# Kernel tuning notes

Measured on AMD Instinct MI355X. Metric: run time of the kernel, lower is better.

## Reference

```python
import jax, jax.numpy as jnp
import numpy as np

NBINS = (128, 64, 32)
LOG2PI = float(np.log(2.0 * np.pi))


def _quadratic_spline_stack(x, genes_oi, local_gene_ix, delta, uh, uw):
    """Stack of piecewise-quadratic (piecewise-linear density) splines on [0,1].
    Per split with n heights / n-1 widths (n-1 bins). Returns (outputs, logabsdet)."""
    uh_oi = uh[genes_oi]  # [G, sum(n)]
    uw_oi = uw[genes_oi]  # [G, sum(n-1)]
    outputs = x
    logabsdet = jnp.zeros_like(x)
    oh = ow = od = 0
    for n in NBINS:
        nh, nw = n, n - 1
        uhs = uh_oi[:, oh:oh + nh]
        uws = uw_oi[:, ow:ow + nw]
        ds = delta[:, od:od + nh]
        oh += nh; ow += nw; od += nh
        # per-gene bin widths / locations
        widths_g = jax.nn.softmax(uws, axis=-1)                     # [G, nw]
        bl = jnp.cumsum(widths_g, axis=-1)
        bl = bl.at[:, -1].set(1.0)
        bin_loc_g = jnp.pad(bl, ((0, 0), (1, 0)))                   # [G, nw+1]
        # gather per cut
        w = widths_g[local_gene_ix]                                 # [N, nw]
        loc = bin_loc_g[local_gene_ix]                              # [N, nw+1]
        # per-cut knot heights: gene baseline + cell/gene delta, normalized to unit area
        h_un = jnp.exp(uhs[local_gene_ix] + ds)                     # [N, nh]
        area = jnp.sum(0.5 * (h_un[:, :-1] + h_un[:, 1:]) * w, axis=-1, keepdims=True)
        h = h_un / area                                             # [N, nh]
        seg = 0.5 * (h[:, :-1] + h[:, 1:]) * w                      # bin masses [N, nw]
        left_cdf = jnp.pad(jnp.cumsum(seg, axis=-1)[:, :-1], ((0, 0), (1, 0)))  # [N, nw]
        # locate bin
        bin_idx = jnp.clip(jnp.sum(outputs[:, None] >= loc, axis=-1) - 1, 0, nw - 1)
        gi = bin_idx[:, None]
        loc_l = jnp.take_along_axis(loc, gi, -1)[:, 0]
        w_b = jnp.take_along_axis(w, gi, -1)[:, 0]
        cdf_l = jnp.take_along_axis(left_cdf, gi, -1)[:, 0]
        h_l = jnp.take_along_axis(h, gi, -1)[:, 0]
        h_r = jnp.take_along_axis(h, gi + 1, -1)[:, 0]
        alpha = (outputs - loc_l) / w_b
        outputs = (0.5 * (h_r - h_l) * w_b) * alpha * alpha + h_l * w_b * alpha + cdf_l
        logabsdet = logabsdet + jnp.log(h_l + (h_r - h_l) * alpha)
    return outputs, logabsdet


def setup_inputs() -> dict:
    key = jax.random.key(0)
    ks = jax.random.split(key, 10)
    B, L, G_total, G_oi, C, N = 512, 16, 20000, 500, 224, 200000
    clustering = jax.random.uniform(ks[0], (B, L), dtype=jnp.float32)
    coordinates = jax.random.uniform(ks[1], (N,), dtype=jnp.float32, minval=1e-4, maxval=1.0 - 1e-4)
    genes_oi = jax.random.randint(ks[2], (G_oi,), 0, G_total)
    local_gene_ix = jax.random.randint(ks[3], (N,), 0, G_oi)
    local_cellxgene_ix = jax.random.randint(ks[4], (N,), 0, B * G_oi)
    localcellxgene_ix = jax.random.randint(ks[5], (N,), 0, B * G_total)
    logit_weight = jax.random.normal(ks[6], (G_total, L, C), dtype=jnp.float32) * 0.01
    rho_weight = jax.random.normal(ks[7], (G_total, L), dtype=jnp.float32) * 0.05
    rho_bias = 1e-5 + (1.0 - 1e-5) * jax.random.uniform(ks[8], (G_total,), dtype=jnp.float32)
    k9, k10 = jax.random.split(ks[9])
    unnormalized_heights = jax.random.normal(k9, (G_total, sum(NBINS)), dtype=jnp.float32) * 0.1
    unnormalized_widths = jax.random.normal(k10, (G_total, sum(n - 1 for n in NBINS)), dtype=jnp.float32) * 0.1
    return dict(clustering=clustering, coordinates=coordinates, genes_oi=genes_oi,
                local_gene_ix=local_gene_ix, local_cellxgene_ix=local_cellxgene_ix,
                localcellxgene_ix=localcellxgene_ix, logit_weight=logit_weight,
                rho_weight=rho_weight, rho_bias=rho_bias,
                unnormalized_heights=unnormalized_heights,
                unnormalized_widths=unnormalized_widths)


def reference(clustering, coordinates, genes_oi, local_gene_ix, local_cellxgene_ix,
              localcellxgene_ix, logit_weight, rho_weight, rho_bias,
              unnormalized_heights, unnormalized_widths):
    B = clustering.shape[0]
    G = genes_oi.shape[0]
    n_total_genes = rho_bias.shape[0]
    # Decoder (n_layers=0 -> nn_output = latent)
    lw_oi = logit_weight[genes_oi]                                   # [G, L, C]
    mixture_delta = jnp.einsum('bl,glc->bgc', clustering, lw_oi)     # [B, G, C]
    rho_delta = clustering @ rho_weight.T                            # [B, G_total]
    rho = jax.nn.softmax(jnp.log(rho_bias)[None, :] + rho_delta, axis=-1)
    rho_cuts = rho.reshape(-1)[localcellxgene_ix]                    # [N]
    md_cuts = mixture_delta.reshape(B * G, -1)[local_cellxgene_ix]   # [N, C]
    _, lik_mixture = _quadratic_spline_stack(coordinates, genes_oi, local_gene_ix,
                                             md_cuts, unnormalized_heights, unnormalized_widths)
    lik_overall = jnp.log(rho_cuts) + jnp.log(jnp.float32(n_total_genes))
    elbo = -jnp.sum(lik_mixture + lik_overall)
    # Normal(0, exp(log_scale=0)=1) regularization log-probs
    def normal_logpdf(v):
        return -0.5 * v * v - 0.5 * LOG2PI
    elbo = elbo - jnp.sum(normal_logpdf(lw_oi))
    elbo = elbo - jnp.sum(normal_logpdf(rho_weight[genes_oi]))
    return elbo
```

## Files before the change

### kernel.cpp

```cpp
#include <hip/hip_runtime.h>
#include <cstddef>

#define LOG2PI_F 1.8378770664093453f

__device__ __forceinline__ float wave_sum(float v) {
#pragma unroll
    for (int o = 32; o >= 1; o >>= 1) v += __shfl_xor(v, o, 64);
    return v;
}

__global__ void k_logrb(const float* __restrict__ rho_bias, float* __restrict__ logrb, int G_total) {
    int g = blockIdx.x * blockDim.x + threadIdx.x;
    if (g < G_total) logrb[g] = __logf(rho_bias[g]);
}

__global__ void k_prep_genes(const int* __restrict__ genes_oi,
                             const float* __restrict__ uh, const float* __restrict__ uw,
                             float* __restrict__ uh_sel, float* __restrict__ w_ws,
                             float* __restrict__ loc_ws) {
    const int g = blockIdx.x;
    const int t = threadIdx.x;
    const int gs = genes_oi[g];

    for (int c = t; c < 224; c += 64) uh_sel[(size_t)g * 224 + c] = uh[(size_t)gs * 224 + c];

    __shared__ float w_s[128];
    int oh = 0, ow = 0;
    const int NH[3] = {128, 64, 32};
    for (int lev = 0; lev < 3; ++lev) {
        const int nh = NH[lev], nw = nh - 1;
        float v0 = (t < nw)      ? uw[(size_t)gs * 221 + ow + t]      : -INFINITY;
        float v1 = (t + 64 < nw) ? uw[(size_t)gs * 221 + ow + t + 64] : -INFINITY;
        float mx = fmaxf(v0, v1);
#pragma unroll
        for (int o = 32; o >= 1; o >>= 1) mx = fmaxf(mx, __shfl_xor(mx, o, 64));
        float e0 = (t < nw)      ? __expf(v0 - mx) : 0.f;
        float e1 = (t + 64 < nw) ? __expf(v1 - mx) : 0.f;
        float sm = wave_sum(e0 + e1);
        float inv = 1.0f / sm;
        float w0 = e0 * inv, w1 = e1 * inv;
        if (t < nw)      { w_s[t]      = w0; w_ws[(size_t)g * 221 + ow + t]      = w0; }
        if (t + 64 < nw) { w_s[t + 64] = w1; w_ws[(size_t)g * 221 + ow + t + 64] = w1; }
        __syncthreads();
        for (int k = t; k < nh; k += 64) {
            float acc = 0.f;
            for (int j = 0; j < k; ++j) acc += w_s[j];
            loc_ws[(size_t)g * 224 + oh + k] = (k == nh - 1) ? 1.0f : acc;
        }
        __syncthreads();
        oh += nh; ow += nw;
    }
}

__global__ void k_prep_lwT(const int* __restrict__ genes_oi,
                           const float* __restrict__ lw, const float* __restrict__ rw,
                           float* __restrict__ lwT, float* __restrict__ pB) {
    const int g = blockIdx.x;
    const int tid = threadIdx.x;
    const int gs = genes_oi[g];
    const float* src = lw + (size_t)gs * 3584;
    float* dst = lwT + (size_t)g * 3584;
    float acc = 0.f;
    if (tid < 224) {
        float vv[16];
#pragma unroll
        for (int l = 0; l < 16; ++l) {
            float v = src[l * 224 + tid];
            vv[l] = v;
            acc = fmaf(v, v, acc);
        }
        float4* d4 = (float4*)(dst + (size_t)tid * 16);
#pragma unroll
        for (int q = 0; q < 4; ++q)
            d4[q] = make_float4(vv[4 * q + 0], vv[4 * q + 1], vv[4 * q + 2], vv[4 * q + 3]);
    }
    if (tid < 16) { float v = rw[(size_t)gs * 16 + tid]; acc = fmaf(v, v, acc); }
    __shared__ float sm[256];
    sm[tid] = acc;
    __syncthreads();
    for (int o = 128; o > 0; o >>= 1) { if (tid < o) sm[tid] += sm[tid + o]; __syncthreads(); }
    if (tid == 0) pB[g] = 0.5f * sm[0] + 0.5f * LOG2PI_F * (3584.0f + 16.0f);
}

__global__ void k_lse(const float* __restrict__ clustering, const float* __restrict__ rw,
                      const float* __restrict__ logrb, float* __restrict__ lse, int G_total) {
    const int b = blockIdx.x;
    const int tid = threadIdx.x;
    __shared__ float cl_s[16];
    if (tid < 16) cl_s[tid] = clustering[(size_t)b * 16 + tid];
    __syncthreads();
    float m = -INFINITY, s = 0.f;
    for (int g = tid; g < G_total; g += blockDim.x) {
        const float4* r4 = (const float4*)(rw + (size_t)g * 16);
        float d = 0.f;
#pragma unroll
        for (int q = 0; q < 4; ++q) {
            float4 v = r4[q];
            d = fmaf(cl_s[4 * q + 0], v.x, d);
            d = fmaf(cl_s[4 * q + 1], v.y, d);
            d = fmaf(cl_s[4 * q + 2], v.z, d);
            d = fmaf(cl_s[4 * q + 3], v.w, d);
        }
        float logit = logrb[g] + d;
        float mn = fmaxf(m, logit);
        s = s * __expf(m - mn) + __expf(logit - mn);
        m = mn;
    }
    __shared__ float ms[256], ss[256];
    ms[tid] = m; ss[tid] = s;
    __syncthreads();
    for (int o = 128; o > 0; o >>= 1) {
        if (tid < o) {
            float m2 = ms[tid + o], s2 = ss[tid + o];
            float mn = fmaxf(ms[tid], m2);
            ss[tid] = ss[tid] * __expf(ms[tid] - mn) + s2 * __expf(m2 - mn);
            ms[tid] = mn;
        }
        __syncthreads();
    }
    if (tid == 0) lse[b] = ms[0] + __logf(ss[0]);
}

__launch_bounds__(256)
__global__ void k_main(const float* __restrict__ coordinates,
                       const int* __restrict__ local_gene_ix,
                       const int* __restrict__ local_cellxgene_ix,
                       const int* __restrict__ localcellxgene_ix,
                       const float* __restrict__ clustering,
                       const float* __restrict__ lwT,
                       const float* __restrict__ rw,
                       const float* __restrict__ logrb,
                       const float* __restrict__ lse,
                       const float* __restrict__ uh_sel,
                       const float* __restrict__ w_ws,
                       const float* __restrict__ loc_ws,
                       float* __restrict__ pA,
                       int N, int G_oi, int G_total) {
    const int tid  = threadIdx.x;
    const int lane = tid & 63;
    const int wid  = tid >> 6;
    const int wglobal = blockIdx.x * 4 + wid;
    const int wstride = gridDim.x * 4;
    const float logGt = __logf((float)G_total);

    float acc = 0.f;

    for (int i = wglobal; i < N; i += wstride) {
        const float x_in = coordinates[i];
        const int g_h = local_gene_ix[i];
        const int lcx = local_cellxgene_ix[i];
        const int lc2 = localcellxgene_ix[i];
        const unsigned b1 = (unsigned)lcx / (unsigned)G_oi;
        const unsigned gm = (unsigned)lcx - b1 * (unsigned)G_oi;
        const unsigned b2 = (unsigned)lc2 / (unsigned)G_total;
        const unsigned gt = (unsigned)lc2 - b2 * (unsigned)G_total;

        float cl[16];
        {
            const float4* c4 = (const float4*)(clustering + (size_t)b1 * 16);
#pragma unroll
            for (int q = 0; q < 4; ++q) {
                float4 v = c4[q];
                cl[4 * q + 0] = v.x; cl[4 * q + 1] = v.y; cl[4 * q + 2] = v.z; cl[4 * q + 3] = v.w;
            }
        }

        const float* lwtg = lwT   + (size_t)gm  * 3584;
        const float* uhg  = uh_sel + (size_t)g_h * 224;
        const float* wg   = w_ws   + (size_t)g_h * 221;
        const float* lg   = loc_ws + (size_t)g_h * 224;

        float x = x_in;
        float lad = 0.f;
        int oh = 0, ow = 0;
        const int NH[3] = {128, 64, 32};
#pragma unroll
        for (int lev = 0; lev < 3; ++lev) {
            const int n = NH[lev];
            const int c0 = lane, c1 = lane + 64;
            const bool a0 = (c0 < n);
            const bool a1 = (n > 64);
            float h0 = 0.f, h1 = 0.f;
            if (a0) {
                const float4* p4 = (const float4*)(lwtg + (size_t)(oh + c0) * 16);
                float d = 0.f;
#pragma unroll
                for (int q = 0; q < 4; ++q) {
                    float4 v = p4[q];
                    d = fmaf(cl[4 * q + 0], v.x, d);
                    d = fmaf(cl[4 * q + 1], v.y, d);
                    d = fmaf(cl[4 * q + 2], v.z, d);
                    d = fmaf(cl[4 * q + 3], v.w, d);
                }
                h0 = __expf(uhg[oh + c0] + d);
            }
            if (a1) {
                const float4* p4 = (const float4*)(lwtg + (size_t)(oh + c1) * 16);
                float d = 0.f;
#pragma unroll
                for (int q = 0; q < 4; ++q) {
                    float4 v = p4[q];
                    d = fmaf(cl[4 * q + 0], v.x, d);
                    d = fmaf(cl[4 * q + 1], v.y, d);
                    d = fmaf(cl[4 * q + 2], v.z, d);
                    d = fmaf(cl[4 * q + 3], v.w, d);
                }
                h1 = __expf(uhg[oh + c1] + d);
            }
            const float h0n = __shfl(h0, (lane + 1) & 63, 64);
            const float h1n = __shfl(h1, (lane + 1) & 63, 64);
            const float h64 = __shfl(h1, 0, 64);

            float segA = 0.f, segB = 0.f;
            if (lane < n - 1) {
                float hr = (lane < 63) ? h0n : h64;
                segA = 0.5f * (h0 + hr) * wg[ow + lane];
            }
            if (a1 && lane < 63) {
                segB = 0.5f * (h1 + h1n) * wg[ow + lane + 64];
            }

            float loc0 = a0 ? lg[oh + c0] : 2.f;
            float loc1 = a1 ? lg[oh + c1] : 2.f;
            unsigned long long bb0 = __ballot(a0 && (x >= loc0));
            unsigned long long bb1 = __ballot(a1 && (x >= loc1));
            int cnt = __popcll(bb0) + __popcll(bb1);
            int bi = min(max(cnt - 1, 0), n - 2);

            float pref = ((lane < bi) ? segA : 0.f) + (((lane + 64) < bi) ? segB : 0.f);
            float area = wave_sum(segA + segB);
            float cdf_raw = wave_sum(pref);

            float hl  = (bi < 64)     ? __shfl(h0, bi, 64)     : __shfl(h1, bi - 64, 64);
            int bip = bi + 1;
            float hr2 = (bip < 64)    ? __shfl(h0, bip, 64)    : __shfl(h1, bip - 64, 64);

            float inv_area = 1.0f / area;
            float loc_l = lg[oh + bi];
            float w_b   = wg[ow + bi];
            float hlr = hl * inv_area, hrr = hr2 * inv_area;
            float alpha = (x - loc_l) / w_b;
            x = 0.5f * (hrr - hlr) * w_b * alpha * alpha + hlr * w_b * alpha + cdf_raw * inv_area;
            lad += __logf(hlr + (hrr - hlr) * alpha);
            oh += n; ow += n - 1;
        }

        float d2 = 0.f;
        {
            const float4* c4 = (const float4*)(clustering + (size_t)b2 * 16);
            const float4* r4 = (const float4*)(rw + (size_t)gt * 16);
#pragma unroll
            for (int q = 0; q < 4; ++q) {
                float4 cv = c4[q], rv = r4[q];
                d2 = fmaf(cv.x, rv.x, d2);
                d2 = fmaf(cv.y, rv.y, d2);
                d2 = fmaf(cv.z, rv.z, d2);
                d2 = fmaf(cv.w, rv.w, d2);
            }
        }
        float lik_ov = logrb[gt] + d2 - lse[b2] + logGt;
        acc += -(lad + lik_ov);
    }

    __shared__ float wsum[4];
    if (lane == 0) wsum[wid] = acc;
    __syncthreads();
    if (tid == 0) pA[blockIdx.x] = wsum[0] + wsum[1] + wsum[2] + wsum[3];
}

__global__ void k_final(const float* __restrict__ pA, const float* __restrict__ pB,
                        float* __restrict__ out, int nA, int nB) {
    const int tid = threadIdx.x;
    float acc = 0.f;
    for (int i = tid; i < nA; i += blockDim.x) acc += pA[i];
    for (int i = tid; i < nB; i += blockDim.x) acc += pB[i];
    __shared__ float sm[256];
    sm[tid] = acc;
    __syncthreads();
    for (int o = 128; o > 0; o >>= 1) { if (tid < o) sm[tid] += sm[tid + o]; __syncthreads(); }
    if (tid == 0) out[0] = sm[0];
}

extern "C" void kernel_launch(void* const* d_in, const int* in_sizes, int n_in,
                              void* d_out, int out_size, void* d_ws, size_t ws_size,
                              hipStream_t stream) {
    const float* clustering        = (const float*)d_in[0];
    const float* coordinates       = (const float*)d_in[1];
    const int*   genes_oi          = (const int*)d_in[2];
    const int*   local_gene_ix     = (const int*)d_in[3];
    const int*   local_cellxgene_ix= (const int*)d_in[4];
    const int*   localcellxgene_ix = (const int*)d_in[5];
    const float* lw                = (const float*)d_in[6];
    const float* rw                = (const float*)d_in[7];
    const float* rho_bias          = (const float*)d_in[8];
    const float* uh                = (const float*)d_in[9];
    const float* uw                = (const float*)d_in[10];

    const int G_total = in_sizes[8];
    const int G_oi    = in_sizes[2];
    const int N       = in_sizes[1];
    const int L       = in_sizes[7] / G_total;
    const int B       = in_sizes[0] / L;
    (void)L;

    const int NBLK = 2048;

    size_t off = 0;
    float* base = (float*)d_ws;
    auto alloc = [&](size_t nfloats) {
        float* p = base + off;
        off += (nfloats + 3) & ~(size_t)3;
        return p;
    };
    float* pA      = alloc(NBLK);
    float* pB      = alloc(G_oi);
    float* lse     = alloc(B);
    float* logrb   = alloc(G_total);
    float* lwT     = alloc((size_t)G_oi * 3584);
    float* uh_sel  = alloc((size_t)G_oi * 224);
    float* w_ws    = alloc((size_t)G_oi * 221);
    float* loc_ws  = alloc((size_t)G_oi * 224);
    (void)ws_size;

    k_logrb<<<(G_total + 255) / 256, 256, 0, stream>>>(rho_bias, logrb, G_total);
    k_prep_genes<<<G_oi, 64, 0, stream>>>(genes_oi, uh, uw, uh_sel, w_ws, loc_ws);
    k_prep_lwT<<<G_oi, 256, 0, stream>>>(genes_oi, lw, rw, lwT, pB);
    k_lse<<<B, 256, 0, stream>>>(clustering, rw, logrb, lse, G_total);
    k_main<<<NBLK, 256, 0, stream>>>(coordinates, local_gene_ix, local_cellxgene_ix,
                                     localcellxgene_ix, clustering, lwT, rw, logrb, lse,
                                     uh_sel, w_ws, loc_ws, pA, N, G_oi, G_total);
    k_final<<<1, 256, 0, stream>>>(pA, pB, (float*)d_out, NBLK, G_oi);
}
```

Baseline: 744.8 us.

## Bucket cuts by gene and evaluate spline per-thread with sequential bin scan

Replaces the one-wave-per-cut spline evaluation with a counting sort of cuts by mixture gene (histogram, scan, scatter) followed by one block per gene, where each thread walks all bins of a cut serially. Gene-side data (heights, half-widths, knot locations) is packed into float4 records and the knot cumulative sum becomes a wave scan. This removes the per-cut cross-lane shuffles and reductions and lets a block share one gene's weight rows through cache. In exchange each thread does about 220 serial dot products and exps, there are several extra launches with atomics, and load balance now depends on how many cuts each gene has.

```diff
diff --git a/kernel.cpp b/kernel.cpp
--- a/kernel.cpp
+++ b/kernel.cpp
@@ -6,6 +6,19 @@
 __device__ __forceinline__ float wave_sum(float v) {
 #pragma unroll
     for (int o = 32; o >= 1; o >>= 1) v += __shfl_xor(v, o, 64);
+    return v;
+}
+__device__ __forceinline__ float wave_max(float v) {
+#pragma unroll
+    for (int o = 32; o >= 1; o >>= 1) v = fmaxf(v, __shfl_xor(v, o, 64));
+    return v;
+}
+__device__ __forceinline__ float wave_scan_incl(float v, int lane) {
+#pragma unroll
+    for (int o = 1; o < 64; o <<= 1) {
+        float t = __shfl_up(v, o, 64);
+        if (lane >= o) v += t;
+    }
     return v;
 }
 
@@ -16,40 +29,42 @@
 
 __global__ void k_prep_genes(const int* __restrict__ genes_oi,
                              const float* __restrict__ uh, const float* __restrict__ uw,
-                             float* __restrict__ uh_sel, float* __restrict__ w_ws,
-                             float* __restrict__ loc_ws) {
+                             float4* __restrict__ pk) {
     const int g = blockIdx.x;
     const int t = threadIdx.x;
     const int gs = genes_oi[g];
-
-    for (int c = t; c < 224; c += 64) uh_sel[(size_t)g * 224 + c] = uh[(size_t)gs * 224 + c];
-
-    __shared__ float w_s[128];
-    int oh = 0, ow = 0;
+    const float* uhg = uh + (size_t)gs * 224;
+    const float* uwg = uw + (size_t)gs * 221;
+    float4* pkg = pk + (size_t)g * 224;
+
     const int NH[3] = {128, 64, 32};
+    const int OH[3] = {0, 128, 192};
+    const int OW[3] = {0, 127, 190};
+    const int SO[3] = {0, 128, 191};
+#pragma unroll
     for (int lev = 0; lev < 3; ++lev) {
-        const int nh = NH[lev], nw = nh - 1;
-        float v0 = (t < nw)      ? uw[(size_t)gs * 221 + ow + t]      : -INFINITY;
-        float v1 = (t + 64 < nw) ? uw[(size_t)gs * 221 + ow + t + 64] : -INFINITY;
-        float mx = fmaxf(v0, v1);
-#pragma unroll
-        for (int o = 32; o >= 1; o >>= 1) mx = fmaxf(mx, __shfl_xor(mx, o, 64));
+        const int nw = NH[lev] - 1;
+        float v0 = (t < nw)      ? uwg[OW[lev] + t]      : -INFINITY;
+        float v1 = (t + 64 < nw) ? uwg[OW[lev] + t + 64] : -INFINITY;
+        float mx = wave_max(fmaxf(v0, v1));
         float e0 = (t < nw)      ? __expf(v0 - mx) : 0.f;
         float e1 = (t + 64 < nw) ? __expf(v1 - mx) : 0.f;
-        float sm = wave_sum(e0 + e1);
-        float inv = 1.0f / sm;
+        float inv = 1.0f / wave_sum(e0 + e1);
         float w0 = e0 * inv, w1 = e1 * inv;
-        if (t < nw)      { w_s[t]      = w0; w_ws[(size_t)g * 221 + ow + t]      = w0; }
-        if (t + 64 < nw) { w_s[t + 64] = w1; w_ws[(size_t)g * 221 + ow + t + 64] = w1; }
-        __syncthreads();
-        for (int k = t; k < nh; k += 64) {
-            float acc = 0.f;
-            for (int j = 0; j < k; ++j) acc += w_s[j];
-            loc_ws[(size_t)g * 224 + oh + k] = (k == nh - 1) ? 1.0f : acc;
-        }
-        __syncthreads();
-        oh += nh; ow += nw;
-    }
+        float i0 = wave_scan_incl(w0, t);
+        float tot0 = __shfl(i0, 63, 64);
+        float i1 = wave_scan_incl(w1, t) + tot0;
+        if (t < nw) {
+            float loc = (t == nw - 1) ? 1.0f : i0;
+            pkg[SO[lev] + t] = make_float4(uhg[OH[lev] + t + 1], 0.5f * w0, loc, 0.f);
+        }
+        if (t + 64 < nw) {
+            int j = t + 64;
+            float loc = (j == nw - 1) ? 1.0f : i1;
+            pkg[SO[lev] + j] = make_float4(uhg[OH[lev] + j + 1], 0.5f * w1, loc, 0.f);
+        }
+    }
+    if (t == 0) pkg[127] = make_float4(uhg[0], uhg[128], uhg[192], 0.f);
 }
 
 __global__ void k_prep_lwT(const int* __restrict__ genes_oi,
@@ -121,39 +136,79 @@
     if (tid == 0) lse[b] = ms[0] + __logf(ss[0]);
 }
 
-__launch_bounds__(256)
-__global__ void k_main(const float* __restrict__ coordinates,
-                       const int* __restrict__ local_gene_ix,
-                       const int* __restrict__ local_cellxgene_ix,
-                       const int* __restrict__ localcellxgene_ix,
-                       const float* __restrict__ clustering,
-                       const float* __restrict__ lwT,
-                       const float* __restrict__ rw,
-                       const float* __restrict__ logrb,
-                       const float* __restrict__ lse,
-                       const float* __restrict__ uh_sel,
-                       const float* __restrict__ w_ws,
-                       const float* __restrict__ loc_ws,
-                       float* __restrict__ pA,
-                       int N, int G_oi, int G_total) {
-    const int tid  = threadIdx.x;
-    const int lane = tid & 63;
-    const int wid  = tid >> 6;
-    const int wglobal = blockIdx.x * 4 + wid;
-    const int wstride = gridDim.x * 4;
+__global__ void k_zero(int* __restrict__ p, int n) {
+    int i = blockIdx.x * blockDim.x + threadIdx.x;
+    if (i < n) p[i] = 0;
+}
+
+__global__ void k_hist(const int* __restrict__ lcx, int* __restrict__ counts, int N, int G_oi) {
+    int i = blockIdx.x * blockDim.x + threadIdx.x;
+    if (i < N) atomicAdd(&counts[(unsigned)lcx[i] % (unsigned)G_oi], 1);
+}
+
+__global__ void k_scan(const int* __restrict__ counts, int* __restrict__ offsets,
+                       int* __restrict__ cursor, int G_oi) {
+    __shared__ int sm[512];
+    const int t = threadIdx.x;
+    int v = (t < G_oi) ? counts[t] : 0;
+    sm[t] = v;
+    __syncthreads();
+    for (int o = 1; o < 512; o <<= 1) {
+        int add = (t >= o) ? sm[t - o] : 0;
+        __syncthreads();
+        sm[t] += add;
+        __syncthreads();
+    }
+    if (t < G_oi) {
+        offsets[t + 1] = sm[t];
+        cursor[t] = sm[t] - v;
+    }
+    if (t == 0) offsets[0] = 0;
+}
+
+__global__ void k_scatter(const float* __restrict__ coord, const int* __restrict__ lgix,
+                          const int* __restrict__ lcx, const int* __restrict__ lc2,
+                          int* __restrict__ cursor,
+                          float* __restrict__ xs, int* __restrict__ b1s,
+                          int* __restrict__ lc2s, int* __restrict__ ghs, int N, int G_oi) {
+    int i = blockIdx.x * blockDim.x + threadIdx.x;
+    if (i >= N) return;
+    unsigned v = (unsigned)lcx[i];
+    unsigned g = v % (unsigned)G_oi;
+    int pos = atomicAdd(&cursor[g], 1);
+    xs[pos]   = coord[i];
+    b1s[pos]  = (int)(v / (unsigned)G_oi);
+    lc2s[pos] = lc2[i];
+    ghs[pos]  = lgix[i];
+}
+
+__launch_bounds__(512, 4)
+__global__ void k_main2(const float* __restrict__ xs, const int* __restrict__ b1s,
+                        const int* __restrict__ lc2s, const int* __restrict__ ghs,
+                        const int* __restrict__ offsets,
+                        const float* __restrict__ clustering,
+                        const float* __restrict__ lwT,
+                        const float4* __restrict__ pk,
+                        const float* __restrict__ rw,
+                        const float* __restrict__ logrb,
+                        const float* __restrict__ lse,
+                        float* __restrict__ pA, int G_oi, int G_total) {
+    const int g = blockIdx.x;
+    const int tid = threadIdx.x;
+    const float* lwg = lwT + (size_t)g * 3584;
+    const int s = offsets[g], e = offsets[g + 1];
     const float logGt = __logf((float)G_total);
-
     float acc = 0.f;
 
-    for (int i = wglobal; i < N; i += wstride) {
-        const float x_in = coordinates[i];
-        const int g_h = local_gene_ix[i];
-        const int lcx = local_cellxgene_ix[i];
-        const int lc2 = localcellxgene_ix[i];
-        const unsigned b1 = (unsigned)lcx / (unsigned)G_oi;
-        const unsigned gm = (unsigned)lcx - b1 * (unsigned)G_oi;
-        const unsigned b2 = (unsigned)lc2 / (unsigned)G_total;
-        const unsigned gt = (unsigned)lc2 - b2 * (unsigned)G_total;
+    for (int base = s; base < e; base += 512) {
+        const int i = base + tid;
+        const bool valid = i < e;
+        const int isafe = valid ? i : s;
+        float x = xs[isafe];
+        const int b1  = b1s[isafe];
+        const int lc2 = lc2s[isafe];
+        const int gh  = ghs[isafe];
+        const float4* pkh = pk + (size_t)gh * 224;
 
         float cl[16];
         {
@@ -164,108 +219,76 @@
                 cl[4 * q + 0] = v.x; cl[4 * q + 1] = v.y; cl[4 * q + 2] = v.z; cl[4 * q + 3] = v.w;
             }
         }
-
-        const float* lwtg = lwT   + (size_t)gm  * 3584;
-        const float* uhg  = uh_sel + (size_t)g_h * 224;
-        const float* wg   = w_ws   + (size_t)g_h * 221;
-        const float* lg   = loc_ws + (size_t)g_h * 224;
-
-        float x = x_in;
+        const float4 uh0 = pkh[127];
+        const float uh0v[3] = {uh0.x, uh0.y, uh0.z};
+
         float lad = 0.f;
-        int oh = 0, ow = 0;
         const int NH[3] = {128, 64, 32};
+        const int OH[3] = {0, 128, 192};
+        const int SO[3] = {0, 128, 191};
 #pragma unroll
         for (int lev = 0; lev < 3; ++lev) {
-            const int n = NH[lev];
-            const int c0 = lane, c1 = lane + 64;
-            const bool a0 = (c0 < n);
-            const bool a1 = (n > 64);
-            float h0 = 0.f, h1 = 0.f;
-            if (a0) {
-                const float4* p4 = (const float4*)(lwtg + (size_t)(oh + c0) * 16);
+            const int nw = NH[lev] - 1;
+            const float* rowbase = lwg + (size_t)OH[lev] * 16;
+            float hp;
+            {
                 float d = 0.f;
 #pragma unroll
-                for (int q = 0; q < 4; ++q) {
-                    float4 v = p4[q];
-                    d = fmaf(cl[4 * q + 0], v.x, d);
-                    d = fmaf(cl[4 * q + 1], v.y, d);
-                    d = fmaf(cl[4 * q + 2], v.z, d);
-                    d = fmaf(cl[4 * q + 3], v.w, d);
-                }
-                h0 = __expf(uhg[oh + c0] + d);
+                for (int l = 0; l < 16; ++l) d = fmaf(cl[l], rowbase[l], d);
+                hp = __expf(uh0v[lev] + d);
             }
-            if (a1) {
-                const float4* p4 = (const float4*)(lwtg + (size_t)(oh + c1) * 16);
+            float h_l = hp, h_r = hp, whb = 0.f, loc_l = 0.f, cdf = 0.f, area = 0.f;
+            int in = 0;
+            const float4* pks = pkh + SO[lev];
+            for (int j = 0; j < nw; ++j) {
+                const float* row = rowbase + (size_t)(j + 1) * 16;
                 float d = 0.f;
 #pragma unroll
-                for (int q = 0; q < 4; ++q) {
-                    float4 v = p4[q];
-                    d = fmaf(cl[4 * q + 0], v.x, d);
-                    d = fmaf(cl[4 * q + 1], v.y, d);
-                    d = fmaf(cl[4 * q + 2], v.z, d);
-                    d = fmaf(cl[4 * q + 3], v.w, d);
-                }
-                h1 = __expf(uhg[oh + c1] + d);
+                for (int l = 0; l < 16; ++l) d = fmaf(cl[l], row[l], d);
+                float4 pkv = pks[j];
+                float hn = __expf(pkv.x + d);
+                float seg = (hp + hn) * pkv.y;
+                bool inJ = (in == j);
+                if (inJ) { h_r = hn; whb = pkv.y; }
+                bool adv = (x >= pkv.z) && (j < nw - 1);
+                if (adv) { cdf += seg; h_l = hn; loc_l = pkv.z; in = j + 1; }
+                area += seg;
+                hp = hn;
             }
-            const float h0n = __shfl(h0, (lane + 1) & 63, 64);
-            const float h1n = __shfl(h1, (lane + 1) & 63, 64);
-            const float h64 = __shfl(h1, 0, 64);
-
-            float segA = 0.f, segB = 0.f;
-            if (lane < n - 1) {
-                float hr = (lane < 63) ? h0n : h64;
-                segA = 0.5f * (h0 + hr) * wg[ow + lane];
-            }
-            if (a1 && lane < 63) {
-                segB = 0.5f * (h1 + h1n) * wg[ow + lane + 64];
-            }
-
-            float loc0 = a0 ? lg[oh + c0] : 2.f;
-            float loc1 = a1 ? lg[oh + c1] : 2.f;
-            unsigned long long bb0 = __ballot(a0 && (x >= loc0));
-            unsigned long long bb1 = __ballot(a1 && (x >= loc1));
-            int cnt = __popcll(bb0) + __popcll(bb1);
-            int bi = min(max(cnt - 1, 0), n - 2);
-
-            float pref = ((lane < bi) ? segA : 0.f) + (((lane + 64) < bi) ? segB : 0.f);
-            float area = wave_sum(segA + segB);
-            float cdf_raw = wave_sum(pref);
-
-            float hl  = (bi < 64)     ? __shfl(h0, bi, 64)     : __shfl(h1, bi - 64, 64);
-            int bip = bi + 1;
-            float hr2 = (bip < 64)    ? __shfl(h0, bip, 64)    : __shfl(h1, bip - 64, 64);
-
-            float inv_area = 1.0f / area;
-            float loc_l = lg[oh + bi];
-            float w_b   = wg[ow + bi];
-            float hlr = hl * inv_area, hrr = hr2 * inv_area;
-            float alpha = (x - loc_l) / w_b;
-            x = 0.5f * (hrr - hlr) * w_b * alpha * alpha + hlr * w_b * alpha + cdf_raw * inv_area;
-            lad += __logf(hlr + (hrr - hlr) * alpha);
-            oh += n; ow += n - 1;
-        }
-
+            float inv_area = __builtin_amdgcn_rcpf(area);
+            float alpha = (x - loc_l) * 0.5f * __builtin_amdgcn_rcpf(whb);
+            float t2 = whb * alpha;
+            x = (t2 * fmaf(h_r - h_l, alpha, 2.f * h_l) + cdf) * inv_area;
+            lad += __logf(fmaf(h_r - h_l, alpha, h_l)) - __logf(area);
+        }
+
+        unsigned b2 = (unsigned)lc2 / (unsigned)G_total;
+        unsigned gt = (unsigned)lc2 - b2 * (unsigned)G_total;
         float d2 = 0.f;
         {
-            const float4* c4 = (const float4*)(clustering + (size_t)b2 * 16);
-            const float4* r4 = (const float4*)(rw + (size_t)gt * 16);
+            const float4* c24 = (const float4*)(clustering + (size_t)b2 * 16);
+            const float4* r4  = (const float4*)(rw + (size_t)gt * 16);
 #pragma unroll
             for (int q = 0; q < 4; ++q) {
-                float4 cv = c4[q], rv = r4[q];
-                d2 = fmaf(cv.x, rv.x, d2);
-                d2 = fmaf(cv.y, rv.y, d2);
-                d2 = fmaf(cv.z, rv.z, d2);
-                d2 = fmaf(cv.w, rv.w, d2);
+                float4 a = c24[q], b = r4[q];
+                d2 = fmaf(a.x, b.x, d2); d2 = fmaf(a.y, b.y, d2);
+                d2 = fmaf(a.z, b.z, d2); d2 = fmaf(a.w, b.w, d2);
             }
         }
-        float lik_ov = logrb[gt] + d2 - lse[b2] + logGt;
-        acc += -(lad + lik_ov);
-    }
-
-    __shared__ float wsum[4];
-    if (lane == 0) wsum[wid] = acc;
-    __syncthreads();
-    if (tid == 0) pA[blockIdx.x] = wsum[0] + wsum[1] + wsum[2] + wsum[3];
+        float lik = logrb[gt] + d2 - lse[b2] + logGt;
+        if (valid) acc -= (lad + lik);
+    }
+
+    acc = wave_sum(acc);
+    __shared__ float wsm[8];
+    if ((tid & 63) == 0) wsm[tid >> 6] = acc;
+    __syncthreads();
+    if (tid == 0) {
+        float t = 0.f;
+#pragma unroll
+        for (int w = 0; w < 8; ++w) t += wsm[w];
+        pA[g] = t;
+    }
 }
 
 __global__ void k_final(const float* __restrict__ pA, const float* __restrict__ pB,
@@ -301,33 +324,41 @@
     const int N       = in_sizes[1];
     const int L       = in_sizes[7] / G_total;
     const int B       = in_sizes[0] / L;
-    (void)L;
-
-    const int NBLK = 2048;
 
     size_t off = 0;
-    float* base = (float*)d_ws;
-    auto alloc = [&](size_t nfloats) {
-        float* p = base + off;
-        off += (nfloats + 3) & ~(size_t)3;
-        return p;
+    char* base = (char*)d_ws;
+    auto alloc = [&](size_t nbytes) {
+        char* p = base + off;
+        off = (off + nbytes + 15) & ~(size_t)15;
+        return (void*)p;
     };
-    float* pA      = alloc(NBLK);
-    float* pB      = alloc(G_oi);
-    float* lse     = alloc(B);
-    float* logrb   = alloc(G_total);
-    float* lwT     = alloc((size_t)G_oi * 3584);
-    float* uh_sel  = alloc((size_t)G_oi * 224);
-    float* w_ws    = alloc((size_t)G_oi * 221);
-    float* loc_ws  = alloc((size_t)G_oi * 224);
+    float*  pA      = (float*)alloc(sizeof(float) * (G_oi + 16));
+    float*  pB      = (float*)alloc(sizeof(float) * (G_oi + 16));
+    float*  lse     = (float*)alloc(sizeof(float) * (B + 16));
+    float*  logrb   = (float*)alloc(sizeof(float) * G_total);
+    float*  lwT     = (float*)alloc(sizeof(float) * (size_t)G_oi * 3584);
+    float4* pk      = (float4*)alloc(sizeof(float4) * (size_t)G_oi * 224);
+    int*    counts  = (int*)alloc(sizeof(int) * 512);
+    int*    offsets = (int*)alloc(sizeof(int) * 512);
+    int*    cursor  = (int*)alloc(sizeof(int) * 512);
+    float*  xs      = (float*)alloc(sizeof(float) * N);
+    int*    b1s     = (int*)alloc(sizeof(int) * N);
+    int*    lc2s    = (int*)alloc(sizeof(int) * N);
+    int*    ghs     = (int*)alloc(sizeof(int) * N);
     (void)ws_size;
 
-    k_logrb<<<(G_total + 255) / 256, 256, 0, stream>>>(rho_bias, logrb, G_total);
-    k_prep_genes<<<G_oi, 64, 0, stream>>>(genes_oi, uh, uw, uh_sel, w_ws, loc_ws);
+    const int TPB = 256;
+    k_logrb<<<(G_total + TPB - 1) / TPB, TPB, 0, stream>>>(rho_bias, logrb, G_total);
+    k_prep_genes<<<G_oi, 64, 0, stream>>>(genes_oi, uh, uw, pk);
     k_prep_lwT<<<G_oi, 256, 0, stream>>>(genes_oi, lw, rw, lwT, pB);
     k_lse<<<B, 256, 0, stream>>>(clustering, rw, logrb, lse, G_total);
-    k_main<<<NBLK, 256, 0, stream>>>(coordinates, local_gene_ix, local_cellxgene_ix,
-                                     localcellxgene_ix, clustering, lwT, rw, logrb, lse,
-                                     uh_sel, w_ws, loc_ws, pA, N, G_oi, G_total);
-    k_final<<<1, 256, 0, stream>>>(pA, pB, (float*)d_out, NBLK, G_oi);
-}
+    k_zero<<<2, 256, 0, stream>>>(counts, 512);
+    k_hist<<<(N + TPB - 1) / TPB, TPB, 0, stream>>>(local_cellxgene_ix, counts, N, G_oi);
+    k_scan<<<1, 512, 0, stream>>>(counts, offsets, cursor, G_oi);
+    k_scatter<<<(N + TPB - 1) / TPB, TPB, 0, stream>>>(coordinates, local_gene_ix,
+                                                       local_cellxgene_ix, localcellxgene_ix,
+                                                       cursor, xs, b1s, lc2s, ghs, N, G_oi);
+    k_main2<<<G_oi, 512, 0, stream>>>(xs, b1s, lc2s, ghs, offsets, clustering, lwT, pk,
+                                      rw, logrb, lse, pA, G_oi, G_total);
+    k_final<<<1, 256, 0, stream>>>(pA, pB, (float*)d_out, G_oi, G_oi);
+}
```

Measured after the change: 674.8 us. 1.1x faster.
